# Kernel tuning notes

Hardware: AMD Instinct MI355X
Metric: run time of the kernel (lower is better)

Reference implementation:

```python
import jax, jax.numpy as jnp
import numpy as np

NF = 64   # num_feat
DG = 8    # deformable_groups (also conv groups)
B, H, W = 4, 96, 96
K = 9     # 3x3 kernel positions


def _conv(x, w, b, padding=1, dilation=1, groups=1):
    out = jax.lax.conv_general_dilated(
        x, w, (1, 1), [(padding, padding), (padding, padding)],
        rhs_dilation=(dilation, dilation),
        dimension_numbers=('NCHW', 'OIHW', 'NCHW'),
        feature_group_count=groups)
    return out + b[None, :, None, None]


def _lrelu(t):
    return jnp.where(t >= 0, t, 0.1 * t)


def _cat_align(a, b):
    # channel-interleaved concat: [a0,b0,a1,b1,...]
    Bn, k, h, w = a.shape
    return jnp.stack([a, b], axis=2).reshape(Bn, 2 * k, h, w)


def _deform_conv(x, offset, mask, weight, bias, dilation, padding):
    # DCNv2 modulated deformable conv, stride 1.
    Bn, C, h, w = x.shape
    Cpg = C // DG
    off = offset.reshape(Bn, DG, K, 2, h, w)          # (dy, dx) per group/kernel pos
    m = mask.reshape(Bn, DG, K, h, w)
    ky = (jnp.repeat(jnp.arange(3), 3) * dilation - padding).astype(x.dtype)  # (K,)
    kx = (jnp.tile(jnp.arange(3), 3) * dilation - padding).astype(x.dtype)
    hs = jnp.arange(h, dtype=x.dtype)
    ws = jnp.arange(w, dtype=x.dtype)
    py = off[:, :, :, 0] + ky[None, None, :, None, None] + hs[None, None, None, :, None]
    px = off[:, :, :, 1] + kx[None, None, :, None, None] + ws[None, None, None, None, :]
    y0f = jnp.floor(py); x0f = jnp.floor(px)
    ly = (py - y0f)[:, :, None]  # broadcast over Cpg
    lx = (px - x0f)[:, :, None]
    y0 = y0f.astype(jnp.int32); x0 = x0f.astype(jnp.int32)
    xg = x.reshape(Bn, DG, Cpg, h * w)

    def gather(yi, xi):
        inb = ((yi >= 0) & (yi < h) & (xi >= 0) & (xi < w))
        idx = (jnp.clip(yi, 0, h - 1) * w + jnp.clip(xi, 0, w - 1)).reshape(Bn, DG, 1, K * h * w)
        v = jnp.take_along_axis(xg, jnp.broadcast_to(idx, (Bn, DG, Cpg, K * h * w)), axis=3)
        return v.reshape(Bn, DG, Cpg, K, h, w) * inb[:, :, None].astype(x.dtype)

    v00 = gather(y0, x0); v01 = gather(y0, x0 + 1)
    v10 = gather(y0 + 1, x0); v11 = gather(y0 + 1, x0 + 1)
    val = (v00 * (1 - ly) * (1 - lx) + v01 * (1 - ly) * lx
           + v10 * ly * (1 - lx) + v11 * ly * lx) * m[:, :, None]
    sampled = val.reshape(Bn, C, K, h, w)
    out = jnp.einsum('bckhw,ock->bohw', sampled, weight.reshape(weight.shape[0], C, K))
    return out + bias[None, :, None, None]


def _dcn(x, off_feat, om_w, om_b, w, b, dilation):
    pad = dilation  # int(3/2)*dilation
    out = _conv(off_feat, om_w, om_b, padding=pad, dilation=dilation)
    o1, o2, msk = jnp.split(out, 3, axis=1)
    offset = jnp.concatenate([o1, o2], axis=1)
    mask = jax.nn.sigmoid(msk)
    return _deform_conv(x, offset, mask, w, b, dilation, pad)


def setup_inputs() -> dict:
    key = jax.random.key(0)
    ks = iter(jax.random.split(key, 64))
    def rn(shape, s=0.05):
        return jax.random.normal(next(ks), shape, jnp.float32) * s
    d = {}
    d['nbr_feat'] = jax.random.normal(next(ks), (B, NF, H, W), jnp.float32)
    d['ref_feat'] = jax.random.normal(next(ks), (B, NF, H, W), jnp.float32)
    for lv, has3 in [('l3', False), ('l2', True), ('l1', True)]:
        d[f'oc1_w_{lv}'] = rn((NF, 2 * NF // DG, 3, 3)); d[f'oc1_b_{lv}'] = rn((NF,))
        oc2_in = 2 * NF if has3 else NF
        d[f'oc2_w_{lv}'] = rn((NF, oc2_in // DG, 3, 3)); d[f'oc2_b_{lv}'] = rn((NF,))
        if has3:
            d[f'oc3_w_{lv}'] = rn((NF, NF // DG, 3, 3)); d[f'oc3_b_{lv}'] = rn((NF,))
            d[f'fc_w_{lv}'] = rn((NF, 2 * NF // DG, 3, 3)); d[f'fc_b_{lv}'] = rn((NF,))
        d[f'om_w_{lv}'] = rn((DG * 3 * K, NF, 3, 3), 0.01); d[f'om_b_{lv}'] = rn((DG * 3 * K,), 0.01)
        d[f'dcn_w_{lv}'] = rn((NF, NF, 3, 3)); d[f'dcn_b_{lv}'] = rn((NF,))
    d['cas_oc1_w'] = rn((NF, 2 * NF // DG, 3, 3)); d['cas_oc1_b'] = rn((NF,))
    d['cas_oc2_w'] = rn((NF, NF // DG, 3, 3)); d['cas_oc2_b'] = rn((NF,))
    d['cas_om_w'] = rn((DG * 3 * K, NF, 3, 3), 0.01); d['cas_om_b'] = rn((DG * 3 * K,), 0.01)
    d['cas_w'] = rn((NF, NF, 3, 3)); d['cas_b'] = rn((NF,))
    return d


def reference(nbr_feat, ref_feat,
              oc1_w_l3, oc1_b_l3, oc2_w_l3, oc2_b_l3, om_w_l3, om_b_l3, dcn_w_l3, dcn_b_l3,
              oc1_w_l2, oc1_b_l2, oc2_w_l2, oc2_b_l2, oc3_w_l2, oc3_b_l2, fc_w_l2, fc_b_l2,
              om_w_l2, om_b_l2, dcn_w_l2, dcn_b_l2,
              oc1_w_l1, oc1_b_l1, oc2_w_l1, oc2_b_l1, oc3_w_l1, oc3_b_l1, fc_w_l1, fc_b_l1,
              om_w_l1, om_b_l1, dcn_w_l1, dcn_b_l1,
              cas_oc1_w, cas_oc1_b, cas_oc2_w, cas_oc2_b, cas_om_w, cas_om_b, cas_w, cas_b):
    # level 3 (dilation 5)
    off = _lrelu(_conv(_cat_align(nbr_feat, ref_feat), oc1_w_l3, oc1_b_l3, groups=DG))
    off = _lrelu(_conv(off, oc2_w_l3, oc2_b_l3, groups=DG))
    feat = _lrelu(_dcn(nbr_feat, off, om_w_l3, om_b_l3, dcn_w_l3, dcn_b_l3, 5))
    to, tf = off, feat
    # level 2 (dilation 3)
    off = _lrelu(_conv(_cat_align(nbr_feat, ref_feat), oc1_w_l2, oc1_b_l2, groups=DG))
    off = _lrelu(_conv(_cat_align(off, to), oc2_w_l2, oc2_b_l2, groups=DG))
    off = _lrelu(_conv(off, oc3_w_l2, oc3_b_l2, groups=DG))
    feat = _dcn(nbr_feat, off, om_w_l2, om_b_l2, dcn_w_l2, dcn_b_l2, 3)
    feat = _lrelu(_conv(_cat_align(feat, tf), fc_w_l2, fc_b_l2, groups=DG))
    to, tf = off, feat
    # level 1 (dilation 1), no lrelu on feat
    off = _lrelu(_conv(_cat_align(nbr_feat, ref_feat), oc1_w_l1, oc1_b_l1, groups=DG))
    off = _lrelu(_conv(_cat_align(off, to), oc2_w_l1, oc2_b_l1, groups=DG))
    off = _lrelu(_conv(off, oc3_w_l1, oc3_b_l1, groups=DG))
    feat = _dcn(nbr_feat, off, om_w_l1, om_b_l1, dcn_w_l1, dcn_b_l1, 1)
    feat = _conv(_cat_align(feat, tf), fc_w_l1, fc_b_l1, groups=DG)
    # cascade
    off = _cat_align(feat, ref_feat)
    off = _lrelu(_conv(_lrelu(_conv(off, cas_oc1_w, cas_oc1_b, groups=DG)), cas_oc2_w, cas_oc2_b, groups=DG))
    feat = _lrelu(_dcn(feat, off, cas_om_w, cas_om_b, cas_w, cas_b, 1))
    return feat
```

## Files before the change

### kernel.cpp

```cpp
#include <hip/hip_runtime.h>

#define BATCH 4
#define NFEAT 64
#define DGRP 8
#define HH 96
#define WW 96
#define HWP (HH*WW)

typedef short short4a __attribute__((ext_vector_type(4)));
typedef short short8 __attribute__((ext_vector_type(8)));
typedef float f32x4 __attribute__((ext_vector_type(4)));
typedef float f32x16 __attribute__((ext_vector_type(16)));

__device__ inline short f2bf(float f) {
  union { float f; unsigned u; } v; v.f = f;
  unsigned r = v.u + 0x7fff + ((v.u >> 16) & 1);
  return (short)(r >> 16);
}
__device__ inline float bf2f(short s) {
  return __uint_as_float(((unsigned)(unsigned short)s) << 16);
}

__device__ __forceinline__ void barrier_keep_vmcnt() {
  asm volatile("s_waitcnt lgkmcnt(0)" ::: "memory");
  __builtin_amdgcn_s_barrier();
  asm volatile("" ::: "memory");
}

struct GwArgs {
  const float* src[12];
  int cat[12];
  int base[13];
};

__device__ __forceinline__ void prep_om_elem(
    int gid, const float* const* s4, short* __restrict__ dst) {
  int t = gid / 147456, r = gid % 147456;
  int tile = r / 18432, r2 = r % 18432;
  int kk = r2 / 512, r3 = r2 % 512;
  int lane = r3 / 8, j = r3 % 8;
  int col = lane & 31, half = lane >> 5;
  int oc = tile * 32 + col;
  int k = kk * 16 + half * 8 + j;
  int p = k >> 6, c = k & 63;
  float v = (oc < 216) ? s4[t][(size_t)oc * 576 + c * 9 + p] : 0.f;
  dst[gid] = f2bf(v);
}

__device__ __forceinline__ void prep_dcnw_elem(
    int gid, const float* const* s4, short* __restrict__ dst) {
  int t = gid / 36864, r = gid % 36864;
  int tile = r / 18432, r2 = r % 18432;
  int kk = r2 / 512, r3 = r2 % 512;
  int lane = r3 / 8, j = r3 % 8;
  int col = lane & 31, half = lane >> 5;
  int oc = tile * 32 + col;
  int k = kk * 16 + half * 8 + j;
  int p = k >> 6, c = k & 63;
  dst[gid] = f2bf(s4[t][(size_t)oc * 576 + c * 9 + p]);
}

__device__ __forceinline__ void prep_gw_elem(
    int gid, const GwArgs& a, short* __restrict__ dst) {
  int t = 0;
  while (gid >= a.base[t + 1]) ++t;
  int r = gid - a.base[t];
  const float* s = a.src[t];
  const int tsz = a.cat[t] ? 4608 : 2560;
  int tile = r / tsz, r2 = r % tsz;
  int kk = r2 / 512, r3 = r2 % 512;
  int lane = r3 >> 3, j = r3 & 7;
  int m = lane & 15, quad = lane >> 4;
  int oc = tile * 16 + m;
  int j32 = quad * 8 + j;
  float val = 0.f;
  if (a.cat[t]) {
    int gsel = j32 >> 4, ssel = (j32 >> 3) & 1, ch8 = j32 & 7;
    if (gsel == (m >> 3)) val = s[oc * 144 + (2 * ch8 + ssel) * 9 + kk];
  } else {
    int tapsel = j32 >> 4, gsel = (j32 >> 3) & 1, ch8 = j32 & 7;
    int p = 2 * kk + tapsel;
    if (p < 9 && gsel == (m >> 3)) val = s[oc * 72 + ch8 * 9 + p];
  }
  dst[gid] = f2bf(val);
}

struct PrepArgs {
  const float* nbr; const float* ref;
  short* nbrT; short* refT;
  const float* omS[4]; short* wbf;
  const float* dwS[4]; short* wdcn;
  GwArgs gw; short* wgc;
};

__global__ __launch_bounds__(256) void prep_fused(PrepArgs a) {
  __shared__ float s[64][65];
  const int bx = blockIdx.x;
  const int lid = threadIdx.x;
  if (bx < 1152) {
    const int x = bx % 144, b = (bx / 144) & 3, z = bx / 576;
    const float* in = z ? a.ref : a.nbr;
    short* out = z ? a.refT : a.nbrT;
    const int p0 = x * 64;
    const int tx = lid & 63, ty = lid >> 6;
    for (int c = ty; c < 64; c += 4)
      s[c][tx] = in[((size_t)b * NFEAT + c) * HWP + p0 + tx];
    __syncthreads();
    for (int p = ty; p < 64; p += 4)
      out[((size_t)b * HWP + p0 + p) * NFEAT + tx] = f2bf(s[tx][p]);
  } else {
    const int gid = (bx - 1152) * 256 + lid;
    if (gid < 589824) prep_om_elem(gid, a.omS, a.wbf);
    else if (gid < 737280) prep_dcnw_elem(gid - 589824, a.dwS, a.wdcn);
    else if (gid < 925696) prep_gw_elem(gid - 737280, a.gw, a.wgc);
  }
}

template <bool CAT, bool LRELU>
__device__ __forceinline__ void gconv_body(
    const short* __restrict__ in0, const short* __restrict__ in1,
    const short* __restrict__ Wsh, const float* __restrict__ bias,
    short* __restrict__ out, int pixbase, int b, int lid) {
  const int lane = lid & 63, t = lid >> 6;
  const int n = lane & 15, quad = lane >> 4;
  constexpr int NKK = CAT ? 9 : 5;

  short8 A[NKK];
#pragma unroll
  for (int kk = 0; kk < NKK; ++kk)
    A[kk] = *(const short8*)(Wsh + ((size_t)(t * NKK + kk) * 64 + lane) * 8);

  const short* sb;
  if (CAT) {
    sb = ((quad & 1) ? in1 : in0) + (size_t)b * HWP * 64 + (2 * t + (quad >> 1)) * 8;
  } else {
    sb = in0 + (size_t)b * HWP * 64 + (2 * t + (quad & 1)) * 8;
  }

  f32x4 acc[2] = {};
#pragma unroll
  for (int nt = 0; nt < 2; ++nt) {
    const int pix = pixbase + nt * 16 + n;
    const int yp = pix / WW, xp = pix % WW;
#pragma unroll
    for (int kk = 0; kk < NKK; ++kk) {
      const int p = CAT ? kk : (2 * kk + (quad >> 1));
      short8 B = {0, 0, 0, 0, 0, 0, 0, 0};
      if (p < 9) {
        const int sy = yp + p / 3 - 1, sx = xp + p % 3 - 1;
        if (((unsigned)sy < (unsigned)HH) && ((unsigned)sx < (unsigned)WW))
          B = *(const short8*)(sb + (size_t)(sy * WW + sx) * 64);
      }
      acc[nt] = __builtin_amdgcn_mfma_f32_16x16x32_bf16(A[kk], B, acc[nt], 0, 0, 0);
    }
  }

  const int ocb = t * 16 + quad * 4;
  const float b0 = bias[ocb], b1 = bias[ocb + 1], b2 = bias[ocb + 2], b3 = bias[ocb + 3];
#pragma unroll
  for (int nt = 0; nt < 2; ++nt) {
    float v0 = acc[nt][0] + b0, v1 = acc[nt][1] + b1;
    float v2 = acc[nt][2] + b2, v3 = acc[nt][3] + b3;
    if (LRELU) {
      v0 = (v0 >= 0.f) ? v0 : 0.1f * v0;
      v1 = (v1 >= 0.f) ? v1 : 0.1f * v1;
      v2 = (v2 >= 0.f) ? v2 : 0.1f * v2;
      v3 = (v3 >= 0.f) ? v3 : 0.1f * v3;
    }
    short4a pk = {f2bf(v0), f2bf(v1), f2bf(v2), f2bf(v3)};
    *(short4a*)(out + ((size_t)b * HWP + pixbase + nt * 16 + n) * 64 + ocb) = pk;
  }
}

template <bool CAT, bool LRELU>
__global__ __launch_bounds__(256) void gconv_mfma(
    const short* __restrict__ in0, const short* __restrict__ in1,
    const short* __restrict__ Wsh, const float* __restrict__ bias,
    short* __restrict__ out) {
  gconv_body<CAT, LRELU>(in0, in1, Wsh, bias, out, blockIdx.x * 32, blockIdx.y,
                         threadIdx.x);
}

struct Oc1Args {
  const short* W[3];
  const float* bias[3];
  short* out[3];
};

__global__ __launch_bounds__(256) void gconv_oc1x3(
    const short* __restrict__ in0, const short* __restrict__ in1, Oc1Args a) {
  const int job = blockIdx.z;
  gconv_body<true, true>(in0, in1, a.W[job], a.bias[job], a.out[job],
                         blockIdx.x * 32, blockIdx.y, threadIdx.x);
}

#define BPITCH 324
template <int D>
__device__ __forceinline__ void omconv_body(
    short* Bs,
    const short* __restrict__ pixT, const short* __restrict__ Wsh,
    const float* __restrict__ bias, short* __restrict__ out,
    int xblk, int b, int lid) {
  const int lane = lid & 63;
  const int w = lid >> 6;
  const int col = lane & 31, half = lane >> 5;
  const int pixbase = xblk * 32;

  const short* aP0 = Wsh + ((size_t)(w * 36) * 64) * 8 + (size_t)lane * 8;
  const short* aP1 = Wsh + ((size_t)((w + 4) * 36) * 64) * 8 + (size_t)lane * 8;
  const short* pixb = pixT + (size_t)b * HWP * 64;

  f32x16 acc00 = {}, acc10 = {};

  for (int i = lid; i < 32 * 5 * 8; i += 256) {
    int row = i / 40, q = i % 40;
    int p = q >> 3, c8 = q & 7;
    int pix = pixbase + row;
    int yp = pix / WW, xp = pix % WW;
    int sy = yp + (p / 3 - 1) * D, sx = xp + (p % 3 - 1) * D;
    short4a lo = {0, 0, 0, 0}, hi = {0, 0, 0, 0};
    if (((unsigned)sy < (unsigned)HH) && ((unsigned)sx < (unsigned)WW)) {
      const short* src = pixb + (size_t)(sy * WW + sx) * 64 + c8 * 8;
      lo = *(const short4a*)src;
      hi = *(const short4a*)(src + 4);
    }
    short* dst = Bs + row * BPITCH + q * 8;
    *(short4a*)dst = lo;
    *(short4a*)(dst + 4) = hi;
  }

  short4a p1lo[4], p1hi[4];
  int p1dst[4];
#pragma unroll
  for (int idx = 0; idx < 4; ++idx) {
    int i = lid + idx * 256;
    int row = i / 32, q = i % 32;
    int p = 5 + (q >> 3), c8 = q & 7;
    int pix = pixbase + row;
    int yp = pix / WW, xp = pix % WW;
    int sy = yp + (p / 3 - 1) * D, sx = xp + (p % 3 - 1) * D;
    short4a lo = {0, 0, 0, 0}, hi = {0, 0, 0, 0};
    if (((unsigned)sy < (unsigned)HH) && ((unsigned)sx < (unsigned)WW)) {
      const short* src = pixb + (size_t)(sy * WW + sx) * 64 + c8 * 8;
      lo = *(const short4a*)src;
      hi = *(const short4a*)(src + 4);
    }
    p1lo[idx] = lo;
    p1hi[idx] = hi;
    p1dst[idx] = row * BPITCH + q * 8;
  }
  barrier_keep_vmcnt();

#pragma unroll 4
  for (int kk = 0; kk < 20; ++kk) {
    short8 A0 = *(const short8*)(aP0 + (size_t)kk * 512);
    short8 A1 = *(const short8*)(aP1 + (size_t)kk * 512);
    const short* b0 = Bs + col * BPITCH + kk * 16 + half * 8;
    short4a l0 = *(const short4a*)b0, h0 = *(const short4a*)(b0 + 4);
    short8 B0 = {l0[0], l0[1], l0[2], l0[3], h0[0], h0[1], h0[2], h0[3]};
    acc00 = __builtin_amdgcn_mfma_f32_32x32x16_bf16(A0, B0, acc00, 0, 0, 0);
    acc10 = __builtin_amdgcn_mfma_f32_32x32x16_bf16(A1, B0, acc10, 0, 0, 0);
  }
  barrier_keep_vmcnt();

#pragma unroll
  for (int idx = 0; idx < 4; ++idx) {
    short* dst = Bs + p1dst[idx];
    *(short4a*)dst = p1lo[idx];
    *(short4a*)(dst + 4) = p1hi[idx];
  }
  barrier_keep_vmcnt();

#pragma unroll 4
  for (int kk = 0; kk < 16; ++kk) {
    const int kkg = 20 + kk;
    short8 A0 = *(const short8*)(aP0 + (size_t)kkg * 512);
    short8 A1 = *(const short8*)(aP1 + (size_t)kkg * 512);
    const short* b0 = Bs + col * BPITCH + kk * 16 + half * 8;
    short4a l0 = *(const short4a*)b0, h0 = *(const short4a*)(b0 + 4);
    short8 B0 = {l0[0], l0[1], l0[2], l0[3], h0[0], h0[1], h0[2], h0[3]};
    acc00 = __builtin_amdgcn_mfma_f32_32x32x16_bf16(A0, B0, acc00, 0, 0, 0);
    acc10 = __builtin_amdgcn_mfma_f32_32x32x16_bf16(A1, B0, acc10, 0, 0, 0);
  }

  const int pix0 = pixbase + col;
#pragma unroll
  for (int r = 0; r < 16; ++r) {
    const int rrow = (r & 3) + 8 * (r >> 2) + 4 * half;
    const int oc0 = w * 32 + rrow;
    const int oc1 = (w + 4) * 32 + rrow;
    out[((size_t)b * 216 + oc0) * HWP + pix0] = f2bf(acc00[r] + bias[oc0]);
    if (oc1 < 216)
      out[((size_t)b * 216 + oc1) * HWP + pix0] = f2bf(acc10[r] + bias[oc1]);
  }
}

template <int D>
__global__ __launch_bounds__(256) void omconv_mfma(
    const short* __restrict__ pixT, const short* __restrict__ Wsh,
    const float* __restrict__ bias, short* __restrict__ out) {
  __shared__ short Bs[32 * BPITCH];
  omconv_body<D>(Bs, pixT, Wsh, bias, out, blockIdx.x, blockIdx.y, threadIdx.x);
}

template <int D, bool LRELU, bool PMOUT>
__device__ __forceinline__ void dcn_body(
    char* smem,
    const short* __restrict__ xT, const short* __restrict__ om,
    const short* __restrict__ Wd, const float* __restrict__ bias,
    void* __restrict__ outv, int pb, int b, int lid) {
  short* Ls = (short*)smem;
  float* red = (float*)smem;
  const int tx = lid & 31, ty = lid >> 5;

  {
    const int px = tx, dg = ty;
    const int pix = pb * 32 + px;
    const int yp = pix / WW, xp = pix % WW;
    const size_t bOM = (size_t)b * 216 * HWP;
    const short* xb = xT + (size_t)b * HWP * 64 + dg * 8;
    short* Sp = Ls + (size_t)((dg & 1) * 32 + px) * 8;

#pragma unroll
    for (int k = 0; k < 9; ++k) {
      float dy = bf2f(om[bOM + (size_t)(dg * 18 + 2 * k) * HWP + pix]);
      float dxv = bf2f(om[bOM + (size_t)(dg * 18 + 2 * k + 1) * HWP + pix]);
      float mr = bf2f(om[bOM + (size_t)(144 + dg * 9 + k) * HWP + pix]);
      float m = 1.f / (1.f + __expf(-mr));
      float py = (float)(yp + (k / 3 - 1) * D) + dy;
      float px_ = (float)(xp + (k % 3 - 1) * D) + dxv;
      float y0f = floorf(py), x0f = floorf(px_);
      float ly = py - y0f, lx = px_ - x0f;
      int y0 = (int)y0f, x0 = (int)x0f;
      int y1 = y0 + 1, x1 = x0 + 1;
      bool vy0 = (unsigned)y0 < (unsigned)HH, vy1 = (unsigned)y1 < (unsigned)HH;
      bool vx0 = (unsigned)x0 < (unsigned)WW, vx1 = (unsigned)x1 < (unsigned)WW;
      int cy0 = min(max(y0, 0), HH - 1), cy1 = min(max(y1, 0), HH - 1);
      int cx0 = min(max(x0, 0), WW - 1), cx1 = min(max(x1, 0), WW - 1);
      float w00 = (vy0 && vx0) ? (1.f - ly) * (1.f - lx) * m : 0.f;
      float w01 = (vy0 && vx1) ? (1.f - ly) * lx * m : 0.f;
      float w10 = (vy1 && vx0) ? ly * (1.f - lx) * m : 0.f;
      float w11 = (vy1 && vx1) ? ly * lx * m : 0.f;
      short8 s00 = *(const short8*)(xb + (size_t)(cy0 * WW + cx0) * 64);
      short8 s01 = *(const short8*)(xb + (size_t)(cy0 * WW + cx1) * 64);
      short8 s10 = *(const short8*)(xb + (size_t)(cy1 * WW + cx0) * 64);
      short8 s11 = *(const short8*)(xb + (size_t)(cy1 * WW + cx1) * 64);
      short8 pk;
#pragma unroll
      for (int cl = 0; cl < 8; ++cl) {
        float v = w00 * bf2f(s00[cl]) + w01 * bf2f(s01[cl]) +
                  w10 * bf2f(s10[cl]) + w11 * bf2f(s11[cl]);
        pk[cl] = f2bf(v);
      }
      const int kk = k * 4 + (dg >> 1);
      *(short8*)(Sp + (size_t)kk * 512) = pk;
    }
  }
  __syncthreads();

  const int lane = lid & 63, w = lid >> 6;
  const int col = lane & 31, half = lane >> 5;
  const int octile = w & 1, kh = w >> 1;
  const int pix = pb * 32 + col;

  const short* aP = Wd + ((size_t)(octile * 36) * 64 + lane) * 8;
  const short* bP = Ls + (size_t)lane * 8;

  f32x16 acc = {};
#pragma unroll 6
  for (int kk = 0; kk < 18; ++kk) {
    const int kkg = kh * 18 + kk;
    short8 A = *(const short8*)(aP + (size_t)kkg * 512);
    short8 B = *(const short8*)(bP + (size_t)kkg * 512);
    acc = __builtin_amdgcn_mfma_f32_32x32x16_bf16(A, B, acc, 0, 0, 0);
  }
  __syncthreads();

  if (kh == 1) {
#pragma unroll
    for (int r = 0; r < 16; ++r) red[((size_t)octile * 64 + lane) * 17 + r] = acc[r];
  }
  __syncthreads();
  if (kh == 0) {
    const float* rp = red + ((size_t)octile * 64 + lane) * 17;
    if (PMOUT) {
      short* out = (short*)outv;
#pragma unroll
      for (int rg = 0; rg < 4; ++rg) {
        short4a pk;
#pragma unroll
        for (int i = 0; i < 4; ++i) {
          const int r = rg * 4 + i;
          const int oc = octile * 32 + i + 8 * rg + 4 * half;
          float v = acc[r] + rp[r] + bias[oc];
          if (LRELU) v = (v >= 0.f) ? v : 0.1f * v;
          pk[i] = f2bf(v);
        }
        *(short4a*)(out + ((size_t)b * HWP + pix) * 64 + octile * 32 + 8 * rg + 4 * half) = pk;
      }
    } else {
      float* out = (float*)outv;
#pragma unroll
      for (int r = 0; r < 16; ++r) {
        const int oc = octile * 32 + (r & 3) + 8 * (r >> 2) + 4 * half;
        float v = acc[r] + rp[r] + bias[oc];
        if (LRELU) v = (v >= 0.f) ? v : 0.1f * v;
        out[((size_t)b * NFEAT + oc) * HWP + pix] = v;
      }
    }
  }
}

template <int D, bool LRELU, bool PMOUT>
__global__ __launch_bounds__(256) void dcn_fused(
    const short* __restrict__ xT, const short* __restrict__ om,
    const short* __restrict__ Wd, const float* __restrict__ bias,
    void* __restrict__ outv) {
  __shared__ __align__(16) char smem[36864];
  dcn_body<D, LRELU, PMOUT>(smem, xT, om, Wd, bias, outv,
                            blockIdx.x, blockIdx.y, threadIdx.x);
}

template <int D>
__global__ __launch_bounds__(256) void om_gc(
    const short* __restrict__ pixT, const short* __restrict__ Wom,
    const float* __restrict__ obias, short* __restrict__ omOut,
    const short* __restrict__ g0, const short* __restrict__ g1,
    const short* __restrict__ gW, const float* __restrict__ gb,
    short* __restrict__ gout) {
  __shared__ short Bs[32 * BPITCH];
  if (blockIdx.x < 288)
    omconv_body<D>(Bs, pixT, Wom, obias, omOut, blockIdx.x, blockIdx.y, threadIdx.x);
  else
    gconv_body<true, true>(g0, g1, gW, gb, gout, (blockIdx.x - 288) * 32,
                           blockIdx.y, threadIdx.x);
}

template <int D, bool DLRELU>
__global__ __launch_bounds__(256) void dcn_gc(
    const short* __restrict__ xT, const short* __restrict__ om,
    const short* __restrict__ Wd, const float* __restrict__ dbias,
    short* __restrict__ dout,
    const short* __restrict__ g0, const short* __restrict__ gW,
    const float* __restrict__ gb, short* __restrict__ gout) {
  __shared__ __align__(16) char smem[36864];
  if (blockIdx.x < 288)
    dcn_body<D, DLRELU, true>(smem, xT, om, Wd, dbias, dout,
                              blockIdx.x, blockIdx.y, threadIdx.x);
  else
    gconv_body<false, true>(g0, nullptr, gW, gb, gout, (blockIdx.x - 288) * 32,
                            blockIdx.y, threadIdx.x);
}

extern "C" void kernel_launch(void* const* d_in, const int* in_sizes, int n_in,
                              void* d_out, int out_size, void* d_ws, size_t ws_size,
                              hipStream_t stream) {
  const float* nbr = (const float*)d_in[0];
  const float* ref = (const float*)d_in[1];
  auto f = [&](int i) { return (const float*)d_in[i]; };

  short* s0 = (short*)d_ws;
  const size_t PM = (size_t)BATCH * HWP * 64;
  short* omB = s0;
  short* refT = omB + 7962624;
  short* pmA = refT + PM;
  short* pmB = pmA + PM;
  short* pmC = pmB + PM;
  short* pmD = pmC + PM;
  short* pmE = pmD + PM;
  short* pmF = pmE + PM;
  short* pmG = pmF + PM;
  short* wbf = pmG + PM;
  short* wdcn = wbf + 589824;
  short* wgc = wdcn + 147456;
  short* nbrT = (short*)d_out;

  static const int gSrc[12] = {2, 4, 10, 12, 14, 16, 22, 24, 26, 28, 34, 36};
  static const int gCat[12] = {1, 0, 1, 1, 0, 1, 1, 1, 0, 1, 1, 0};
  GwArgs ga;
  int gb = 0;
  const short* wg[12];
  for (int t = 0; t < 12; ++t) {
    ga.src[t] = f(gSrc[t]);
    ga.cat[t] = gCat[t];
    ga.base[t] = gb;
    wg[t] = wgc + gb;
    gb += gCat[t] ? 18432 : 10240;
  }
  ga.base[12] = gb;

  PrepArgs pa;
  pa.nbr = nbr; pa.ref = ref; pa.nbrT = nbrT; pa.refT = refT;
  pa.omS[0] = f(6);  pa.omS[1] = f(18); pa.omS[2] = f(30); pa.omS[3] = f(38);
  pa.wbf = wbf;
  pa.dwS[0] = f(8);  pa.dwS[1] = f(20); pa.dwS[2] = f(32); pa.dwS[3] = f(40);
  pa.wdcn = wdcn;
  pa.gw = ga; pa.wgc = wgc;
  prep_fused<<<dim3(4768), 256, 0, stream>>>(pa);

  short* wbf_l3 = wbf;
  short* wbf_l2 = wbf + 147456;
  short* wbf_l1 = wbf + 2 * 147456;
  short* wbf_cas = wbf + 3 * 147456;
  short* wd_l3 = wdcn;
  short* wd_l2 = wdcn + 36864;
  short* wd_l1 = wdcn + 2 * 36864;
  short* wd_cas = wdcn + 3 * 36864;

  dim3 gcGrid(288, BATCH);
  dim3 oc1Grid(288, BATCH, 3);
  dim3 omgcGrid(576, BATCH);
  dim3 dcngcGrid(576, BATCH);
  dim3 omGrid(288, BATCH);
  dim3 dfGrid(288, BATCH);

  Oc1Args oa;
  oa.W[0] = wg[0]; oa.bias[0] = f(3);  oa.out[0] = pmA;
  oa.W[1] = wg[2]; oa.bias[1] = f(11); oa.out[1] = pmF;
  oa.W[2] = wg[6]; oa.bias[2] = f(23); oa.out[2] = pmG;
  gconv_oc1x3<<<oc1Grid, 256, 0, stream>>>(nbrT, refT, oa);

  gconv_mfma<false, true><<<gcGrid, 256, 0, stream>>>(pmA, nullptr, wg[1], f(5), pmB);

  om_gc<5><<<omgcGrid, 256, 0, stream>>>(pmB, wbf_l3, f(7), omB,
                                         pmF, pmB, wg[3], f(13), pmD);
  dcn_gc<5, true><<<dcngcGrid, 256, 0, stream>>>(nbrT, omB, wd_l3, f(9), pmC,
                                                 pmD, wg[4], f(15), pmE);
  om_gc<3><<<omgcGrid, 256, 0, stream>>>(pmE, wbf_l2, f(19), omB,
                                         pmG, pmE, wg[7], f(25), pmB);
  dcn_gc<3, false><<<dcngcGrid, 256, 0, stream>>>(nbrT, omB, wd_l2, f(21), pmD,
                                                  pmB, wg[8], f(27), pmF);
  om_gc<1><<<omgcGrid, 256, 0, stream>>>(pmF, wbf_l1, f(31), omB,
                                         pmD, pmC, wg[5], f(17), pmA);
  dcn_fused<1, false, true><<<dfGrid, 256, 0, stream>>>(nbrT, omB, wd_l1, f(33), pmE);
  gconv_mfma<true, false><<<gcGrid, 256, 0, stream>>>(pmE, pmA, wg[9], f(29), pmB);

  gconv_mfma<true, true><<<gcGrid, 256, 0, stream>>>(pmB, refT, wg[10], f(35), pmC);
  gconv_mfma<false, true><<<gcGrid, 256, 0, stream>>>(pmC, nullptr, wg[11], f(37), pmD);
  omconv_mfma<1><<<omGrid, 256, 0, stream>>>(pmD, wbf_cas, f(39), omB);
  dcn_fused<1, true, false><<<dfGrid, 256, 0, stream>>>(pmB, omB, wd_cas, f(41), (float*)d_out);
}
```

Baseline: 507.3 us.

## Split DCN sampling into two K-phases to halve shared memory

```diff
diff --git a/kernel.cpp b/kernel.cpp
--- a/kernel.cpp
+++ b/kernel.cpp
@@ -313,69 +313,80 @@
   float* red = (float*)smem;
   const int tx = lid & 31, ty = lid >> 5;
 
-  {
-    const int px = tx, dg = ty;
-    const int pix = pb * 32 + px;
-    const int yp = pix / WW, xp = pix % WW;
-    const size_t bOM = (size_t)b * 216 * HWP;
-    const short* xb = xT + (size_t)b * HWP * 64 + dg * 8;
-    short* Sp = Ls + (size_t)((dg & 1) * 32 + px) * 8;
-
-#pragma unroll
-    for (int k = 0; k < 9; ++k) {
-      float dy = bf2f(om[bOM + (size_t)(dg * 18 + 2 * k) * HWP + pix]);
-      float dxv = bf2f(om[bOM + (size_t)(dg * 18 + 2 * k + 1) * HWP + pix]);
-      float mr = bf2f(om[bOM + (size_t)(144 + dg * 9 + k) * HWP + pix]);
-      float m = 1.f / (1.f + __expf(-mr));
-      float py = (float)(yp + (k / 3 - 1) * D) + dy;
-      float px_ = (float)(xp + (k % 3 - 1) * D) + dxv;
-      float y0f = floorf(py), x0f = floorf(px_);
-      float ly = py - y0f, lx = px_ - x0f;
-      int y0 = (int)y0f, x0 = (int)x0f;
-      int y1 = y0 + 1, x1 = x0 + 1;
-      bool vy0 = (unsigned)y0 < (unsigned)HH, vy1 = (unsigned)y1 < (unsigned)HH;
-      bool vx0 = (unsigned)x0 < (unsigned)WW, vx1 = (unsigned)x1 < (unsigned)WW;
-      int cy0 = min(max(y0, 0), HH - 1), cy1 = min(max(y1, 0), HH - 1);
-      int cx0 = min(max(x0, 0), WW - 1), cx1 = min(max(x1, 0), WW - 1);
-      float w00 = (vy0 && vx0) ? (1.f - ly) * (1.f - lx) * m : 0.f;
-      float w01 = (vy0 && vx1) ? (1.f - ly) * lx * m : 0.f;
-      float w10 = (vy1 && vx0) ? ly * (1.f - lx) * m : 0.f;
-      float w11 = (vy1 && vx1) ? ly * lx * m : 0.f;
-      short8 s00 = *(const short8*)(xb + (size_t)(cy0 * WW + cx0) * 64);
-      short8 s01 = *(const short8*)(xb + (size_t)(cy0 * WW + cx1) * 64);
-      short8 s10 = *(const short8*)(xb + (size_t)(cy1 * WW + cx0) * 64);
-      short8 s11 = *(const short8*)(xb + (size_t)(cy1 * WW + cx1) * 64);
-      short8 pk;
-#pragma unroll
-      for (int cl = 0; cl < 8; ++cl) {
-        float v = w00 * bf2f(s00[cl]) + w01 * bf2f(s01[cl]) +
-                  w10 * bf2f(s10[cl]) + w11 * bf2f(s11[cl]);
-        pk[cl] = f2bf(v);
-      }
-      const int kk = k * 4 + (dg >> 1);
-      *(short8*)(Sp + (size_t)kk * 512) = pk;
+  const int dg = ty;
+  const int pixS = pb * 32 + tx;
+  const int ypS = pixS / WW, xpS = pixS % WW;
+  const size_t bOM = (size_t)b * 216 * HWP;
+  const short* xb = xT + (size_t)b * HWP * 64 + dg * 8;
+  short* Sp = Ls + (size_t)((dg & 1) * 32 + tx) * 8;
+
+  auto sample_k = [&](int k, int slotbase) {
+    float dy = bf2f(om[bOM + (size_t)(dg * 18 + 2 * k) * HWP + pixS]);
+    float dxv = bf2f(om[bOM + (size_t)(dg * 18 + 2 * k + 1) * HWP + pixS]);
+    float mr = bf2f(om[bOM + (size_t)(144 + dg * 9 + k) * HWP + pixS]);
+    float m = 1.f / (1.f + __expf(-mr));
+    float py = (float)(ypS + (k / 3 - 1) * D) + dy;
+    float px_ = (float)(xpS + (k % 3 - 1) * D) + dxv;
+    float y0f = floorf(py), x0f = floorf(px_);
+    float ly = py - y0f, lx = px_ - x0f;
+    int y0 = (int)y0f, x0 = (int)x0f;
+    int y1 = y0 + 1, x1 = x0 + 1;
+    bool vy0 = (unsigned)y0 < (unsigned)HH, vy1 = (unsigned)y1 < (unsigned)HH;
+    bool vx0 = (unsigned)x0 < (unsigned)WW, vx1 = (unsigned)x1 < (unsigned)WW;
+    int cy0 = min(max(y0, 0), HH - 1), cy1 = min(max(y1, 0), HH - 1);
+    int cx0 = min(max(x0, 0), WW - 1), cx1 = min(max(x1, 0), WW - 1);
+    float w00 = (vy0 && vx0) ? (1.f - ly) * (1.f - lx) * m : 0.f;
+    float w01 = (vy0 && vx1) ? (1.f - ly) * lx * m : 0.f;
+    float w10 = (vy1 && vx0) ? ly * (1.f - lx) * m : 0.f;
+    float w11 = (vy1 && vx1) ? ly * lx * m : 0.f;
+    short8 s00 = *(const short8*)(xb + (size_t)(cy0 * WW + cx0) * 64);
+    short8 s01 = *(const short8*)(xb + (size_t)(cy0 * WW + cx1) * 64);
+    short8 s10 = *(const short8*)(xb + (size_t)(cy1 * WW + cx0) * 64);
+    short8 s11 = *(const short8*)(xb + (size_t)(cy1 * WW + cx1) * 64);
+    short8 pk;
+#pragma unroll
+    for (int cl = 0; cl < 8; ++cl) {
+      float v = w00 * bf2f(s00[cl]) + w01 * bf2f(s01[cl]) +
+                w10 * bf2f(s10[cl]) + w11 * bf2f(s11[cl]);
+      pk[cl] = f2bf(v);
     }
-  }
-  __syncthreads();
+    const int slot = k * 4 + (dg >> 1) - slotbase;
+    *(short8*)(Sp + (size_t)slot * 512) = pk;
+  };
 
   const int lane = lid & 63, w = lid >> 6;
   const int col = lane & 31, half = lane >> 5;
   const int octile = w & 1, kh = w >> 1;
-  const int pix = pb * 32 + col;
-
   const short* aP = Wd + ((size_t)(octile * 36) * 64 + lane) * 8;
   const short* bP = Ls + (size_t)lane * 8;
-
   f32x16 acc = {};
-#pragma unroll 6
-  for (int kk = 0; kk < 18; ++kk) {
-    const int kkg = kh * 18 + kk;
+
+#pragma unroll
+  for (int k = 0; k < 5; ++k) sample_k(k, 0);
+  __syncthreads();
+#pragma unroll
+  for (int i = 0; i < 10; ++i) {
+    const int kkg = kh * 10 + i;
     short8 A = *(const short8*)(aP + (size_t)kkg * 512);
     short8 B = *(const short8*)(bP + (size_t)kkg * 512);
     acc = __builtin_amdgcn_mfma_f32_32x32x16_bf16(A, B, acc, 0, 0, 0);
   }
   __syncthreads();
 
+#pragma unroll
+  for (int k = 5; k < 9; ++k) sample_k(k, 20);
+  __syncthreads();
+#pragma unroll
+  for (int i = 0; i < 8; ++i) {
+    const int kkg = 20 + kh * 8 + i;
+    const int kkl = kh * 8 + i;
+    short8 A = *(const short8*)(aP + (size_t)kkg * 512);
+    short8 B = *(const short8*)(bP + (size_t)kkl * 512);
+    acc = __builtin_amdgcn_mfma_f32_32x32x16_bf16(A, B, acc, 0, 0, 0);
+  }
+  __syncthreads();
+
+  const int pix = pb * 32 + col;
   if (kh == 1) {
 #pragma unroll
     for (int r = 0; r < 16; ++r) red[((size_t)octile * 64 + lane) * 17 + r] = acc[r];
@@ -412,11 +423,11 @@
 }
 
 template <int D, bool LRELU, bool PMOUT>
-__global__ __launch_bounds__(256) void dcn_fused(
+__global__ __launch_bounds__(256, 8) void dcn_fused(
     const short* __restrict__ xT, const short* __restrict__ om,
     const short* __restrict__ Wd, const float* __restrict__ bias,
     void* __restrict__ outv) {
-  __shared__ __align__(16) char smem[36864];
+  __shared__ __align__(16) char smem[20480];
   dcn_body<D, LRELU, PMOUT>(smem, xT, om, Wd, bias, outv,
                             blockIdx.x, blockIdx.y, threadIdx.x);
 }
@@ -437,13 +448,13 @@
 }
 
 template <int D, bool DLRELU>
-__global__ __launch_bounds__(256) void dcn_gc(
+__global__ __launch_bounds__(256, 8) void dcn_gc(
     const short* __restrict__ xT, const short* __restrict__ om,
     const short* __restrict__ Wd, const float* __restrict__ dbias,
     short* __restrict__ dout,
     const short* __restrict__ g0, const short* __restrict__ gW,
     const float* __restrict__ gb, short* __restrict__ gout) {
-  __shared__ __align__(16) char smem[36864];
+  __shared__ __align__(16) char smem[20480];
   if (blockIdx.x < 288)
     dcn_body<D, DLRELU, true>(smem, xT, om, Wd, dbias, dout,
                               blockIdx.x, blockIdx.y, threadIdx.x);
```

After: 512.7 us. About the same (+1.1%).

## Store offset/mask in pixel-major padded layout for vector loads in DCN

Applied to the files above, without the earlier changes.

```diff
diff --git a/kernel.cpp b/kernel.cpp
--- a/kernel.cpp
+++ b/kernel.cpp
@@ -195,6 +195,7 @@
 }
 
 #define BPITCH 324
+#define TPITCH 264
 template <int D>
 __device__ __forceinline__ void omconv_body(
     short* Bs,
@@ -283,15 +284,30 @@
     acc10 = __builtin_amdgcn_mfma_f32_32x32x16_bf16(A1, B0, acc10, 0, 0, 0);
   }
 
-  const int pix0 = pixbase + col;
+  __syncthreads();
+  short* LsT = Bs;
 #pragma unroll
   for (int r = 0; r < 16; ++r) {
     const int rrow = (r & 3) + 8 * (r >> 2) + 4 * half;
     const int oc0 = w * 32 + rrow;
+    const int dg0 = oc0 / 18, idx0 = oc0 % 18;
+    LsT[col * TPITCH + dg0 * 32 + idx0] = f2bf(acc00[r] + bias[oc0]);
     const int oc1 = (w + 4) * 32 + rrow;
-    out[((size_t)b * 216 + oc0) * HWP + pix0] = f2bf(acc00[r] + bias[oc0]);
-    if (oc1 < 216)
-      out[((size_t)b * 216 + oc1) * HWP + pix0] = f2bf(acc10[r] + bias[oc1]);
+    if (oc1 < 216) {
+      int dg1, idx1;
+      if (oc1 < 144) { dg1 = oc1 / 18; idx1 = oc1 % 18; }
+      else           { dg1 = (oc1 - 144) / 9; idx1 = 18 + (oc1 - 144) % 9; }
+      LsT[col * TPITCH + dg1 * 32 + idx1] = f2bf(acc10[r] + bias[oc1]);
+    }
+  }
+  __syncthreads();
+  const size_t obase = ((size_t)b * HWP + pixbase) * 256;
+#pragma unroll
+  for (int c = 0; c < 4; ++c) {
+    int i = lid + c * 256;
+    int px = i >> 5, part = i & 31;
+    *(short8*)(out + obase + (size_t)px * 256 + part * 8) =
+        *(const short8*)(LsT + px * TPITCH + part * 8);
   }
 }
 
@@ -317,15 +333,23 @@
     const int px = tx, dg = ty;
     const int pix = pb * 32 + px;
     const int yp = pix / WW, xp = pix % WW;
-    const size_t bOM = (size_t)b * 216 * HWP;
     const short* xb = xT + (size_t)b * HWP * 64 + dg * 8;
     short* Sp = Ls + (size_t)((dg & 1) * 32 + px) * 8;
 
+    const short* omp = om + (((size_t)b * HWP + pix) * 8 + dg) * 32;
+    short8 q0 = *(const short8*)(omp);
+    short8 q1 = *(const short8*)(omp + 8);
+    short8 q2 = *(const short8*)(omp + 16);
+    short8 q3 = *(const short8*)(omp + 24);
+
 #pragma unroll
     for (int k = 0; k < 9; ++k) {
-      float dy = bf2f(om[bOM + (size_t)(dg * 18 + 2 * k) * HWP + pix]);
-      float dxv = bf2f(om[bOM + (size_t)(dg * 18 + 2 * k + 1) * HWP + pix]);
-      float mr = bf2f(om[bOM + (size_t)(144 + dg * 9 + k) * HWP + pix]);
+      short dys = (k < 4) ? q0[2 * k] : ((k < 8) ? q1[2 * k - 8] : q2[0]);
+      short dxs = (k < 4) ? q0[2 * k + 1] : ((k < 8) ? q1[2 * k - 7] : q2[1]);
+      short mrs = (k < 6) ? q2[2 + k] : q3[k - 6];
+      float dy = bf2f(dys);
+      float dxv = bf2f(dxs);
+      float mr = bf2f(mrs);
       float m = 1.f / (1.f + __expf(-mr));
       float py = (float)(yp + (k / 3 - 1) * D) + dy;
       float px_ = (float)(xp + (k % 3 - 1) * D) + dxv;
@@ -412,7 +436,7 @@
 }
 
 template <int D, bool LRELU, bool PMOUT>
-__global__ __launch_bounds__(256) void dcn_fused(
+__global__ __launch_bounds__(256, 4) void dcn_fused(
     const short* __restrict__ xT, const short* __restrict__ om,
     const short* __restrict__ Wd, const float* __restrict__ bias,
     void* __restrict__ outv) {
@@ -437,7 +461,7 @@
 }
 
 template <int D, bool DLRELU>
-__global__ __launch_bounds__(256) void dcn_gc(
+__global__ __launch_bounds__(256, 4) void dcn_gc(
     const short* __restrict__ xT, const short* __restrict__ om,
     const short* __restrict__ Wd, const float* __restrict__ dbias,
     short* __restrict__ dout,
@@ -462,7 +486,7 @@
   short* s0 = (short*)d_ws;
   const size_t PM = (size_t)BATCH * HWP * 64;
   short* omB = s0;
-  short* refT = omB + 7962624;
+  short* refT = omB + 9437184;
   short* pmA = refT + PM;
   short* pmB = pmA + PM;
   short* pmC = pmB + PM;
```

After: 506.0 us. No clear change (-0.3%).
